# Kernel optimization log

Hardware: AMD Instinct MI355X
Metric: run time of the kernel (lower is better)

## Reference

```python
import jax, jax.numpy as jnp
from jax import lax
import numpy as np

ARG_NAMES = ('x w1 b1 bn1_g bn1_b bn1_m bn1_v w2 b2 bn2_g bn2_b bn2_m bn2_v w3 b3 w4 b4 '
             'attn_w attn_b attn_u g0_w1 g0_b1 g0_w2 g0_b2 g1_w1 g1_b1 g1_w2 g1_b2 '
             'g2_w1 g2_b1 g2_w2 g2_b2 c_w1 c_b1 c_w2 c_b2 c_w3 c_b3 c_w4 c_b4').split()


def _conv1d(x, w, b, stride, pad):
    # x: [N, C, L], w: [O, I, K]
    y = lax.conv_general_dilated(x, w, (stride,), [(pad, pad)],
                                 dimension_numbers=('NCH', 'OIH', 'NCH'))
    return y + b[None, :, None]


def _bn(x, g, b, m, v, eps=1e-5):
    # eval-mode BatchNorm1d over channel dim of [N, C, L]
    inv = g / jnp.sqrt(v + eps)
    return (x - m[None, :, None]) * inv[None, :, None] + b[None, :, None]


def _forward(x, w1, b1, bn1_g, bn1_b, bn1_m, bn1_v, w2, b2, bn2_g, bn2_b, bn2_m, bn2_v,
             w3, b3, w4, b4, attn_w, attn_b, attn_u,
             g0_w1, g0_b1, g0_w2, g0_b2, g1_w1, g1_b1, g1_w2, g1_b2,
             g2_w1, g2_b1, g2_w2, g2_b2,
             c_w1, c_b1, c_w2, c_b2, c_w3, c_b3, c_w4, c_b4):
    B, S, C, T = x.shape  # [batch, crops, channels=64, time=400]
    h = x.reshape(-1, C, T)
    # CNN stack (dropout = identity in eval)
    h = _bn(jax.nn.elu(_conv1d(h, w1, b1, 2, 1)), bn1_g, bn1_b, bn1_m, bn1_v)   # [N,64,192]
    h = _bn(jax.nn.elu(_conv1d(h, w2, b2, 2, 0)), bn2_g, bn2_b, bn2_m, bn2_v)   # [N,64,87]
    h = jax.nn.elu(_conv1d(h, w3, b3, 1, 0))                                    # [N,64,82]
    h = lax.reduce_window(h, 0.0, lax.add, (1, 1, 3), (1, 1, 2), 'VALID') / 3.0  # [N,64,40]
    h = jax.nn.elu(_conv1d(h, w4, b4, 1, 0))                                    # [N,64,35]
    h = h.reshape(B, S, C, -1)  # [B, S, 64, 35]
    # Attention pooling over the crop dim (dim=1), sum=True
    v = jnp.tanh(jnp.einsum('bsch,hd->bscd', h, attn_w) + attn_b)
    alphas = jax.nn.softmax(jnp.einsum('bscd,d->bsc', v, attn_u), axis=1)
    h = jax.nn.elu((h * alphas[..., None]).sum(axis=1))  # [B, 64, 35]
    # GIN over complete 64-node graph (self-loops included, eps=0):
    # aggregation per node == sum over all nodes of the graph
    def gin(h, W1, B1, W2, B2):
        agg = h + h.sum(axis=1, keepdims=True)
        return jax.nn.relu(agg @ W1 + B1) @ W2 + B2
    h = jax.nn.relu(gin(h, g0_w1, g0_b1, g0_w2, g0_b2))
    h = jax.nn.relu(gin(h, g1_w1, g1_b1, g1_w2, g1_b2))
    h = gin(h, g2_w1, g2_b1, g2_w2, g2_b2)  # no act after last layer
    # Classifier
    f = h.reshape(B, -1)  # [B, 2240]
    f = jax.nn.elu(f @ c_w1 + c_b1)
    f = jax.nn.elu(f @ c_w2 + c_b2)
    f = jax.nn.elu(f @ c_w3 + c_b3)
    return f @ c_w4 + c_b4  # [B, 2]


def setup_inputs() -> dict:
    key = jax.random.key(0)
    ks = iter(jax.random.split(key, 64))
    def rn(shape, s=0.05):
        return jax.random.normal(next(ks), shape, dtype=jnp.float32) * s
    d = {}
    d['x'] = jax.random.normal(next(ks), (32, 16, 64, 400), dtype=jnp.float32)
    d['w1'] = rn((64, 64, 20)); d['b1'] = rn((64,))
    d['bn1_g'] = jnp.ones((64,), jnp.float32); d['bn1_b'] = jnp.zeros((64,), jnp.float32)
    d['bn1_m'] = jnp.zeros((64,), jnp.float32); d['bn1_v'] = jnp.ones((64,), jnp.float32)
    d['w2'] = rn((64, 64, 20)); d['b2'] = rn((64,))
    d['bn2_g'] = jnp.ones((64,), jnp.float32); d['bn2_b'] = jnp.zeros((64,), jnp.float32)
    d['bn2_m'] = jnp.zeros((64,), jnp.float32); d['bn2_v'] = jnp.ones((64,), jnp.float32)
    d['w3'] = rn((64, 64, 6)); d['b3'] = rn((64,))
    d['w4'] = rn((64, 64, 6)); d['b4'] = rn((64,))
    d['attn_w'] = rn((35, 256), 0.1); d['attn_b'] = rn((256,), 0.1); d['attn_u'] = rn((256,), 0.1)
    d['g0_w1'] = rn((35, 256)); d['g0_b1'] = rn((256,))
    d['g0_w2'] = rn((256, 256)); d['g0_b2'] = rn((256,))
    d['g1_w1'] = rn((256, 256)); d['g1_b1'] = rn((256,))
    d['g1_w2'] = rn((256, 256)); d['g1_b2'] = rn((256,))
    d['g2_w1'] = rn((256, 35)); d['g2_b1'] = rn((35,))
    d['g2_w2'] = rn((35, 35)); d['g2_b2'] = rn((35,))
    d['c_w1'] = rn((2240, 256)); d['c_b1'] = rn((256,))
    d['c_w2'] = rn((256, 64)); d['c_b2'] = rn((64,))
    d['c_w3'] = rn((64, 16)); d['c_b3'] = rn((16,))
    d['c_w4'] = rn((16, 2)); d['c_b4'] = rn((2,))
    return d


def reference(x, w1, b1, bn1_g, bn1_b, bn1_m, bn1_v, w2, b2, bn2_g, bn2_b, bn2_m, bn2_v,
              w3, b3, w4, b4, attn_w, attn_b, attn_u,
              g0_w1, g0_b1, g0_w2, g0_b2, g1_w1, g1_b1, g1_w2, g1_b2,
              g2_w1, g2_b1, g2_w2, g2_b2,
              c_w1, c_b1, c_w2, c_b2, c_w3, c_b3, c_w4, c_b4):
    return _forward(x, w1, b1, bn1_g, bn1_b, bn1_m, bn1_v, w2, b2, bn2_g, bn2_b, bn2_m, bn2_v,
                    w3, b3, w4, b4, attn_w, attn_b, attn_u,
                    g0_w1, g0_b1, g0_w2, g0_b2, g1_w1, g1_b1, g1_w2, g1_b2,
                    g2_w1, g2_b1, g2_w2, g2_b2,
                    c_w1, c_b1, c_w2, c_b2, c_w3, c_b3, c_w4, c_b4)
```

## Files before the change

kernel.cpp:

```cpp
#include <hip/hip_runtime.h>
#include <math.h>

typedef __attribute__((ext_vector_type(8))) __bf16 bf16x8;
typedef __attribute__((ext_vector_type(4))) __bf16 bf16x4;
typedef __attribute__((ext_vector_type(4))) float f32x4;

__device__ __forceinline__ float elu_f(float v) {
    return v > 0.f ? v : (expf(v) - 1.f);
}

__global__ __launch_bounds__(256) void prep_all(
    const float* __restrict__ w1, const float* __restrict__ w2,
    const float* __restrict__ w3, const float* __restrict__ w4,
    __bf16* __restrict__ t1, __bf16* __restrict__ t2,
    __bf16* __restrict__ t3, __bf16* __restrict__ t4,
    const float* __restrict__ g0w1, const float* __restrict__ g0w2,
    const float* __restrict__ g1w1, const float* __restrict__ g1w2,
    const float* __restrict__ g2w1, const float* __restrict__ g2w2,
    __bf16* __restrict__ d0, __bf16* __restrict__ d1, __bf16* __restrict__ d2,
    __bf16* __restrict__ d3, __bf16* __restrict__ d4, __bf16* __restrict__ d5)
{
    __shared__ float tl[64][68];
    const int bigbid = blockIdx.x;
    if (bigbid < 832) {
        int idx = bigbid * 256 + threadIdx.x;
        if (idx < 81920) {
            int k = idx / 4096, r = idx - k * 4096, co = r >> 6, ci = r & 63;
            t1[idx] = (__bf16)w1[(co * 64 + ci) * 20 + k];
        } else if (idx < 163840) {
            int j = idx - 81920;
            int k = j / 4096, r = j - k * 4096, co = r >> 6, ci = r & 63;
            t2[j] = (__bf16)w2[(co * 64 + ci) * 20 + k];
        } else if (idx < 188416) {
            int j = idx - 163840;
            int k = j / 4096, r = j - k * 4096, co = r >> 6, ci = r & 63;
            t3[j] = (__bf16)w3[(co * 64 + ci) * 6 + k];
        } else if (idx < 212992) {
            int j = idx - 188416;
            int k = j / 4096, r = j - k * 4096, co = r >> 6, ci = r & 63;
            t4[j] = (__bf16)w4[(co * 64 + ci) * 6 + k];
        }
        return;
    }
    int bid = bigbid - 832;
    const float* src; __bf16* dst; int K, O, Kpad, Opad, tile;
    if (bid < 4)       { src = g0w1; dst = d0; K = 35;   O = 256; Kpad = 64;   Opad = 256; tile = bid; }
    else if (bid < 20) { src = g0w2; dst = d1; K = 256;  O = 256; Kpad = 256;  Opad = 256; tile = bid - 4; }
    else if (bid < 36) { src = g1w1; dst = d2; K = 256;  O = 256; Kpad = 256;  Opad = 256; tile = bid - 20; }
    else if (bid < 52) { src = g1w2; dst = d3; K = 256;  O = 256; Kpad = 256;  Opad = 256; tile = bid - 36; }
    else if (bid < 56) { src = g2w1; dst = d4; K = 256;  O = 35;  Kpad = 256;  Opad = 64;  tile = bid - 52; }
    else               { src = g2w2; dst = d5; K = 35;   O = 35;  Kpad = 64;   Opad = 64;  tile = 0; }
    int ktiles = Kpad >> 6;
    int ot = tile / ktiles, kt = tile - ot * ktiles;
    int k0 = kt * 64, o0 = ot * 64;
    size_t LOFF = (size_t)Opad * Kpad;
    int c = threadIdx.x & 63, rr = threadIdx.x >> 6;
    #pragma unroll
    for (int it = 0; it < 16; ++it) {
        int r = rr + it * 4;
        int kk = k0 + r, oo = o0 + c;
        tl[r][c] = (kk < K && oo < O) ? src[(size_t)kk * O + oo] : 0.f;
    }
    __syncthreads();
    #pragma unroll
    for (int it = 0; it < 16; ++it) {
        int r = rr + it * 4;
        float v = tl[c][r];
        __bf16 hi = (__bf16)v;
        float lo = v - (float)hi;
        size_t pos = (size_t)(o0 + r) * Kpad + k0 + c;
        dst[pos] = hi;
        dst[LOFF + pos] = (__bf16)lo;
    }
}

__global__ __launch_bounds__(512, 2) void conv1234_fused(
    const float* __restrict__ x, const __bf16* __restrict__ wT1,
    const float* __restrict__ b1,
    const float* __restrict__ bn1g, const float* __restrict__ bn1b,
    const float* __restrict__ bn1m, const float* __restrict__ bn1v,
    const __bf16* __restrict__ wT2, const float* __restrict__ b2,
    const float* __restrict__ bn2g, const float* __restrict__ bn2b,
    const float* __restrict__ bn2m, const float* __restrict__ bn2v,
    const __bf16* __restrict__ wT3, const float* __restrict__ b3,
    const __bf16* __restrict__ wT4, const float* __restrict__ b4,
    __bf16* __restrict__ h4)
{
    constexpr int LIN = 400, PAD = 1;
    constexpr int ROWS = 201;
    __shared__ __align__(16) __bf16 smem[2 * ROWS * 72];
    __shared__ __align__(16) __bf16 sw[2 * 64 * 72];

    __bf16* sx   = smem;
    __bf16* bufA = smem;
    __bf16* bufB = smem + 2 * 96 * 72;

    const int tid = threadIdx.x;
    const int n = blockIdx.x;
    const int wave = tid >> 6, lane = tid & 63;
    const int m = lane & 15, quad = lane >> 4;

    {
        const float* xg = x + (size_t)n * 64 * LIN;
        if (tid < 128) {
            int v = (tid >> 6) ? 401 : 0;
            sx[((v & 1) * ROWS + (v >> 1)) * 72 + (tid & 63)] = (__bf16)0.f;
        }
        constexpr int ITEMS = 16 * (LIN / 4);
        #pragma unroll
        for (int it = 0; it < 4; ++it) {
            int idx = it * 512 + tid;
            if (idx < ITEMS) {
                int jj = idx & 3;
                int g  = (idx >> 2) & 15;
                int q  = (idx >> 6) * 4 + jj;
                const float* xp = xg + (size_t)(4 * g) * LIN + 4 * q;
                float fa[4][4];
                #pragma unroll
                for (int u = 0; u < 4; ++u)
                    *(float4*)&fa[u][0] = *(const float4*)(xp + (size_t)u * LIN);
                #pragma unroll
                for (int e = 0; e < 4; ++e) {
                    int v = 4 * q + e + PAD;
                    bf16x4 wv = { (__bf16)fa[0][e], (__bf16)fa[1][e],
                                  (__bf16)fa[2][e], (__bf16)fa[3][e] };
                    *(bf16x4*)&sx[((v & 1) * ROWS + (v >> 1)) * 72 + 4 * g] = wv;
                }
            }
        }
    }

    const int tile = wave >> 1;
    const int coh  = (wave & 1) * 32;
    {
        f32x4 acc[3][2];
        #pragma unroll
        for (int mi = 0; mi < 3; ++mi)
            #pragma unroll
            for (int nj = 0; nj < 2; ++nj)
                acc[mi][nj] = (f32x4){0.f, 0.f, 0.f, 0.f};

        for (int kb = 0; kb < 20; kb += 2) {
            if (kb) __syncthreads();
            #pragma unroll
            for (int i = 0; i < 2; ++i) {
                int idx = i * 512 + tid;
                int r = idx >> 3, p = idx & 7;
                *(uint4*)(sw + (size_t)r * 72 + p * 8) =
                    *(const uint4*)(wT1 + (size_t)(kb + (r >> 6)) * 4096 + (r & 63) * 64 + p * 8);
            }
            __syncthreads();

            #pragma unroll
            for (int kp2 = 0; kp2 < 2; ++kp2) {
                const int kp = kb + kp2;
                const int buf = kp & 1, rowoff = kp >> 1;
                const __bf16* abase = sx + ((size_t)buf * ROWS + tile * 48 + m + rowoff) * 72;
                const __bf16* bbase = sw + (size_t)(kp2 * 64 + coh + m) * 72;
                #pragma unroll
                for (int s = 0; s < 2; ++s) {
                    bf16x8 af[3], bfr[2];
                    #pragma unroll
                    for (int mi = 0; mi < 3; ++mi)
                        af[mi] = *(const bf16x8*)(abase + mi * (16 * 72) + s * 32 + quad * 8);
                    #pragma unroll
                    for (int nj = 0; nj < 2; ++nj)
                        bfr[nj] = *(const bf16x8*)(bbase + nj * (16 * 72) + s * 32 + quad * 8);
                    #pragma unroll
                    for (int mi = 0; mi < 3; ++mi)
                        #pragma unroll
                        for (int nj = 0; nj < 2; ++nj)
                            acc[mi][nj] = __builtin_amdgcn_mfma_f32_16x16x32_bf16(
                                af[mi], bfr[nj], acc[mi][nj], 0, 0, 0);
                }
            }
        }
        __syncthreads();

        #pragma unroll
        for (int nj = 0; nj < 2; ++nj) {
            const int co = coh + nj * 16 + m;
            const float bi = b1[co];
            const float inv   = bn1g[co] / sqrtf(bn1v[co] + 1e-5f);
            const float shift = bn1b[co] - bn1m[co] * inv;
            #pragma unroll
            for (int mi = 0; mi < 3; ++mi)
                #pragma unroll
                for (int r = 0; r < 4; ++r) {
                    int t = tile * 48 + mi * 16 + quad * 4 + r;
                    float v = elu_f(acc[mi][nj][r] + bi) * inv + shift;
                    bufA[((size_t)(t & 1) * 96 + (t >> 1)) * 72 + co] = (__bf16)v;
                }
        }
    }
    __syncthreads();

    const int th  = wave >> 2;
    const int coq = wave & 3;
    {
        f32x4 acc[3];
        #pragma unroll
        for (int mi = 0; mi < 3; ++mi) acc[mi] = (f32x4){0.f, 0.f, 0.f, 0.f};

        for (int kb = 0; kb < 20; kb += 2) {
            __syncthreads();
            #pragma unroll
            for (int i = 0; i < 2; ++i) {
                int idx = i * 512 + tid;
                int r = idx >> 3, p = idx & 7;
                *(uint4*)(sw + (size_t)r * 72 + p * 8) =
                    *(const uint4*)(wT2 + (size_t)(kb + (r >> 6)) * 4096 + (r & 63) * 64 + p * 8);
            }
            __syncthreads();

            #pragma unroll
            for (int kp2 = 0; kp2 < 2; ++kp2) {
                const int kp = kb + kp2;
                const int buf = kp & 1, rowoff = kp >> 1;
                const int r0 = th * 48 + m + rowoff;
                const __bf16* bbase = sw + (size_t)(kp2 * 64 + coq * 16 + m) * 72;
                #pragma unroll
                for (int s = 0; s < 2; ++s) {
                    bf16x8 af[3], bfr;
                    #pragma unroll
                    for (int mi = 0; mi < 3; ++mi) {
                        int rr = r0 + mi * 16; if (rr > 95) rr = 95;
                        af[mi] = *(const bf16x8*)(bufA + ((size_t)buf * 96 + rr) * 72 + s * 32 + quad * 8);
                    }
                    bfr = *(const bf16x8*)(bbase + s * 32 + quad * 8);
                    #pragma unroll
                    for (int mi = 0; mi < 3; ++mi)
                        acc[mi] = __builtin_amdgcn_mfma_f32_16x16x32_bf16(
                            af[mi], bfr, acc[mi], 0, 0, 0);
                }
            }
        }

        const int co = coq * 16 + m;
        const float bi = b2[co];
        float inv = bn2g[co] / sqrtf(bn2v[co] + 1e-5f);
        float shift = bn2b[co] - bn2m[co] * inv;
        #pragma unroll
        for (int mi = 0; mi < 3; ++mi)
            #pragma unroll
            for (int r = 0; r < 4; ++r) {
                int t = th * 48 + mi * 16 + quad * 4 + r;
                if (t < 87) {
                    float v = elu_f(acc[mi][r] + bi) * inv + shift;
                    bufB[t * 72 + co] = (__bf16)v;
                }
            }
    }
    __syncthreads();

    {
        const __bf16* wb = wT3 + (size_t)(coq * 16 + m) * 64 + quad * 8;
        bf16x8 bw[6][2];
        #pragma unroll
        for (int kp = 0; kp < 6; ++kp)
            #pragma unroll
            for (int s = 0; s < 2; ++s)
                bw[kp][s] = *(const bf16x8*)(wb + (size_t)kp * 4096 + s * 32);

        f32x4 acc[3];
        #pragma unroll
        for (int mi = 0; mi < 3; ++mi) acc[mi] = (f32x4){0.f, 0.f, 0.f, 0.f};

        #pragma unroll
        for (int kp = 0; kp < 6; ++kp) {
            const int r0 = th * 48 + m + kp;
            #pragma unroll
            for (int s = 0; s < 2; ++s) {
                bf16x8 af[3];
                #pragma unroll
                for (int mi = 0; mi < 3; ++mi) {
                    int rr = r0 + mi * 16; if (rr > 86) rr = 86;
                    af[mi] = *(const bf16x8*)(bufB + (size_t)rr * 72 + s * 32 + quad * 8);
                }
                #pragma unroll
                for (int mi = 0; mi < 3; ++mi)
                    acc[mi] = __builtin_amdgcn_mfma_f32_16x16x32_bf16(
                        af[mi], bw[kp][s], acc[mi], 0, 0, 0);
            }
        }

        const int co = coq * 16 + m;
        const float bi = b3[co];
        #pragma unroll
        for (int mi = 0; mi < 3; ++mi)
            #pragma unroll
            for (int r = 0; r < 4; ++r) {
                int t = th * 48 + mi * 16 + quad * 4 + r;
                if (t < 82)
                    bufA[(size_t)t * 72 + co] = (__bf16)elu_f(acc[mi][r] + bi);
            }
    }
    __syncthreads();

    #pragma unroll
    for (int it = 0; it < 5; ++it) {
        int idx = it * 512 + tid;
        int t = idx >> 6, co = idx & 63;
        float v = ((float)bufA[(2 * t) * 72 + co] + (float)bufA[(2 * t + 1) * 72 + co] +
                   (float)bufA[(2 * t + 2) * 72 + co]) * (1.f / 3.f);
        bufB[t * 72 + co] = (__bf16)v;
    }
    __syncthreads();

    if (wave < 4) {
        const int co0 = wave * 16;
        const __bf16* wb = wT4 + (size_t)(co0 + m) * 64 + quad * 8;
        bf16x8 bw[6][2];
        #pragma unroll
        for (int kp = 0; kp < 6; ++kp)
            #pragma unroll
            for (int s = 0; s < 2; ++s)
                bw[kp][s] = *(const bf16x8*)(wb + (size_t)kp * 4096 + s * 32);

        f32x4 acc4[3];
        #pragma unroll
        for (int mi = 0; mi < 3; ++mi) acc4[mi] = (f32x4){0.f, 0.f, 0.f, 0.f};

        #pragma unroll
        for (int kp = 0; kp < 6; ++kp) {
            const int r0 = m + kp;
            #pragma unroll
            for (int s = 0; s < 2; ++s) {
                bf16x8 af[3];
                #pragma unroll
                for (int mi = 0; mi < 3; ++mi) {
                    int rr = r0 + mi * 16; if (rr > 39) rr = 39;
                    af[mi] = *(const bf16x8*)(bufB + (size_t)rr * 72 + s * 32 + quad * 8);
                }
                #pragma unroll
                for (int mi = 0; mi < 3; ++mi)
                    acc4[mi] = __builtin_amdgcn_mfma_f32_16x16x32_bf16(
                        af[mi], bw[kp][s], acc4[mi], 0, 0, 0);
            }
        }

        const int co = co0 + m;
        const float bi = b4[co];
        #pragma unroll
        for (int mi = 0; mi < 3; ++mi)
            #pragma unroll
            for (int r = 0; r < 4; ++r) {
                int t = mi * 16 + quad * 4 + r;
                if (t < 35)
                    h4[((size_t)n * 35 + t) * 64 + co] = (__bf16)elu_f(acc4[mi][r] + bi);
            }
    }
}

__global__ __launch_bounds__(256) void attn_pool_k(
    const __bf16* __restrict__ h, const float* __restrict__ W,
    const float* __restrict__ ab, const float* __restrict__ u,
    float* __restrict__ out)
{
    __shared__ float sW[35 * 256];
    __shared__ float sh[4][16 * 35 + 5];
    const int tid = threadIdx.x;
    const int pair0 = blockIdx.x * 4;
    for (int i = tid; i < 35 * 256; i += 256) sW[i] = W[i];
    for (int i = tid; i < 4 * 560; i += 256) {
        int q = i / 560, r = i - q * 560;
        int s = r / 35, t = r - s * 35;
        int bc = pair0 + q, b = bc >> 6, c = bc & 63;
        sh[q][s * 35 + t] = (float)h[(((size_t)b * 16 + s) * 35 + t) * 64 + c];
    }
    __syncthreads();

    const int wave = tid >> 6, lane = tid & 63;
    const int bc = pair0 + wave;
    const float* shw = sh[wave];

    float myu[4], myb[4];
    #pragma unroll
    for (int p = 0; p < 4; ++p) { myu[p] = u[lane + 64 * p]; myb[p] = ab[lane + 64 * p]; }

    float dot[16][4];
    #pragma unroll
    for (int s = 0; s < 16; ++s)
        #pragma unroll
        for (int p = 0; p < 4; ++p) dot[s][p] = myb[p];

    for (int t = 0; t < 35; ++t) {
        float w0 = sW[t * 256 + lane];
        float w1 = sW[t * 256 + lane + 64];
        float w2 = sW[t * 256 + lane + 128];
        float w3 = sW[t * 256 + lane + 192];
        #pragma unroll
        for (int s = 0; s < 16; ++s) {
            float hv = shw[s * 35 + t];
            dot[s][0] = fmaf(hv, w0, dot[s][0]);
            dot[s][1] = fmaf(hv, w1, dot[s][1]);
            dot[s][2] = fmaf(hv, w2, dot[s][2]);
            dot[s][3] = fmaf(hv, w3, dot[s][3]);
        }
    }

    float sc[16];
    #pragma unroll
    for (int s = 0; s < 16; ++s) {
        float v = tanhf(dot[s][0]) * myu[0] + tanhf(dot[s][1]) * myu[1]
                + tanhf(dot[s][2]) * myu[2] + tanhf(dot[s][3]) * myu[3];
        #pragma unroll
        for (int off = 1; off < 64; off <<= 1) v += __shfl_xor(v, off, 64);
        sc[s] = v;
    }

    float mx = sc[0];
    #pragma unroll
    for (int s = 1; s < 16; ++s) mx = fmaxf(mx, sc[s]);
    float e[16], sum = 0.f;
    #pragma unroll
    for (int s = 0; s < 16; ++s) { e[s] = expf(sc[s] - mx); sum += e[s]; }
    float inv = 1.f / sum;

    if (lane < 35) {
        float acc = 0.f;
        #pragma unroll
        for (int s = 0; s < 16; ++s) acc = fmaf(shw[s * 35 + lane], e[s] * inv, acc);
        out[(size_t)bc * 35 + lane] = elu_f(acc);
    }
}

#define APLANE (64 * 264)

__device__ __forceinline__ void gin_gemm_dev(
    const __bf16* As,
    const __bf16* __restrict__ Wg, int Kpad, int wlo, int Kout,
    const float* __restrict__ bias,
    int mode, __bf16* Ad, float* __restrict__ outg)
{
    const int lane = threadIdx.x & 63;
    const int wave = threadIdx.x >> 6;
    const int o0 = wave * 32;
    if (o0 >= ((Kout + 63) & ~63)) return;
    const int m = lane & 15, quad = lane >> 4;

    f32x4 acc[4][2];
    #pragma unroll
    for (int mi = 0; mi < 4; ++mi)
        #pragma unroll
        for (int nj = 0; nj < 2; ++nj)
            acc[mi][nj] = (f32x4){0.f, 0.f, 0.f, 0.f};

    for (int k0 = 0; k0 < Kpad; k0 += 32) {
        bf16x8 ah[4], al[4], bh[2], bl[2];
        #pragma unroll
        for (int mi = 0; mi < 4; ++mi) {
            const __bf16* ap = As + (size_t)(mi * 16 + m) * 264 + k0 + quad * 8;
            ah[mi] = *(const bf16x8*)ap;
            al[mi] = *(const bf16x8*)(ap + APLANE);
        }
        #pragma unroll
        for (int nj = 0; nj < 2; ++nj) {
            const __bf16* wp = Wg + (size_t)(o0 + nj * 16 + m) * Kpad + k0 + quad * 8;
            bh[nj] = *(const bf16x8*)wp;
            bl[nj] = *(const bf16x8*)(wp + wlo);
        }
        #pragma unroll
        for (int mi = 0; mi < 4; ++mi)
            #pragma unroll
            for (int nj = 0; nj < 2; ++nj) {
                acc[mi][nj] = __builtin_amdgcn_mfma_f32_16x16x32_bf16(
                    al[mi], bh[nj], acc[mi][nj], 0, 0, 0);
                acc[mi][nj] = __builtin_amdgcn_mfma_f32_16x16x32_bf16(
                    ah[mi], bl[nj], acc[mi][nj], 0, 0, 0);
                acc[mi][nj] = __builtin_amdgcn_mfma_f32_16x16x32_bf16(
                    ah[mi], bh[nj], acc[mi][nj], 0, 0, 0);
            }
    }

    #pragma unroll
    for (int nj = 0; nj < 2; ++nj) {
        const int o = o0 + nj * 16 + m;
        const bool ovalid = (o < Kout);
        const float bi = ovalid ? bias[o] : 0.f;
        float v[4][4];
        #pragma unroll
        for (int mi = 0; mi < 4; ++mi)
            #pragma unroll
            for (int r = 0; r < 4; ++r)
                v[mi][r] = acc[mi][nj][r] + bi;
        if (mode == 2) {
            if (ovalid) {
                #pragma unroll
                for (int mi = 0; mi < 4; ++mi)
                    #pragma unroll
                    for (int r = 0; r < 4; ++r)
                        outg[(size_t)(mi * 16 + quad * 4 + r) * Kout + o] = v[mi][r];
            }
        } else {
            float s = 0.f;
            #pragma unroll
            for (int mi = 0; mi < 4; ++mi)
                #pragma unroll
                for (int r = 0; r < 4; ++r) {
                    float rv = ovalid ? fmaxf(v[mi][r], 0.f) : 0.f;
                    v[mi][r] = rv;
                    s += rv;
                }
            if (mode == 1) {
                s += __shfl_xor(s, 16, 64);
                s += __shfl_xor(s, 32, 64);
            } else {
                s = 0.f;
            }
            #pragma unroll
            for (int mi = 0; mi < 4; ++mi)
                #pragma unroll
                for (int r = 0; r < 4; ++r) {
                    float a = v[mi][r] + s;
                    __bf16 hi = (__bf16)a;
                    size_t pos = (size_t)(mi * 16 + quad * 4 + r) * 264 + o;
                    Ad[pos] = hi;
                    Ad[APLANE + pos] = (__bf16)(a - (float)hi);
                }
        }
    }
}

__global__ __launch_bounds__(512) void gin_fused(
    const float* __restrict__ ha,
    const __bf16* __restrict__ gW0a, const __bf16* __restrict__ gW0b,
    const __bf16* __restrict__ gW1a, const __bf16* __restrict__ gW1b,
    const __bf16* __restrict__ gW2a, const __bf16* __restrict__ gW2b,
    const float* __restrict__ b0a, const float* __restrict__ b0b,
    const float* __restrict__ b1a, const float* __restrict__ b1b,
    const float* __restrict__ b2a, const float* __restrict__ b2b,
    float* __restrict__ H3)
{
    const int b = blockIdx.x, tid = threadIdx.x;
    __shared__ __align__(16) __bf16 sA[2][2 * APLANE];
    __shared__ float sS[64];
    const float* hab = ha + (size_t)b * 2240;

    if (tid < 64) {
        float s = 0.f;
        if (tid < 35)
            for (int n = 0; n < 64; ++n) s += hab[n * 35 + tid];
        sS[tid] = s;
    }
    __syncthreads();
    for (int idx = tid; idx < 64 * 64; idx += 512) {
        int n = idx >> 6, k = idx & 63;
        float a = (k < 35) ? hab[n * 35 + k] + sS[k] : 0.f;
        __bf16 hi = (__bf16)a;
        sA[0][n * 264 + k] = hi;
        sA[0][APLANE + n * 264 + k] = (__bf16)(a - (float)hi);
    }
    __syncthreads();

    gin_gemm_dev(sA[0], gW0a, 64,  16384, 256, b0a, 0, sA[1], nullptr); __syncthreads();
    gin_gemm_dev(sA[1], gW0b, 256, 65536, 256, b0b, 1, sA[0], nullptr); __syncthreads();
    gin_gemm_dev(sA[0], gW1a, 256, 65536, 256, b1a, 0, sA[1], nullptr); __syncthreads();
    gin_gemm_dev(sA[1], gW1b, 256, 65536, 256, b1b, 1, sA[0], nullptr); __syncthreads();
    gin_gemm_dev(sA[0], gW2a, 256, 16384, 35,  b2a, 0, sA[1], nullptr); __syncthreads();
    gin_gemm_dev(sA[1], gW2b, 64,  4096,  35,  b2b, 2, nullptr, H3 + (size_t)b * 2240);
}

__global__ __launch_bounds__(256) void cls1_part_k(
    const float* __restrict__ H3, const float* __restrict__ w1,
    float* __restrict__ s1p)
{
    const int b  = blockIdx.x;
    const int kc = blockIdx.y;
    const int k0 = kc * 140;
    __shared__ float sH[140];
    const int tid = threadIdx.x;
    if (tid < 140) sH[tid] = H3[(size_t)b * 2240 + k0 + tid];
    __syncthreads();
    const int o = (tid >> 6) * 64 + (tid & 63);
    float a0 = 0.f, a1 = 0.f, a2 = 0.f, a3 = 0.f;
    const float* wr = w1 + (size_t)k0 * 256 + o;
    #pragma unroll
    for (int k = 0; k < 140; k += 4) {
        a0 = fmaf(sH[k],     wr[(size_t)k * 256],       a0);
        a1 = fmaf(sH[k + 1], wr[(size_t)(k + 1) * 256], a1);
        a2 = fmaf(sH[k + 2], wr[(size_t)(k + 2) * 256], a2);
        a3 = fmaf(sH[k + 3], wr[(size_t)(k + 3) * 256], a3);
    }
    s1p[((size_t)kc * 32 + b) * 256 + o] = a0 + a1 + a2 + a3;
}

__global__ __launch_bounds__(256) void cls234_k(
    const float* __restrict__ s1p, const float* __restrict__ b1,
    const float* __restrict__ w2, const float* __restrict__ b2,
    const float* __restrict__ w3, const float* __restrict__ b3,
    const float* __restrict__ w4, const float* __restrict__ b4,
    float* __restrict__ out)
{
    const int b = blockIdx.x, tid = threadIdx.x;
    __shared__ float s1[256];
    __shared__ float part[4][64];
    __shared__ float s2[64];
    __shared__ float s3[16];
    {
        float acc = b1[tid];
        #pragma unroll
        for (int kc = 0; kc < 16; ++kc)
            acc += s1p[((size_t)kc * 32 + b) * 256 + tid];
        s1[tid] = elu_f(acc);
    }
    __syncthreads();
    {
        int kg = tid >> 6, o = tid & 63;
        float acc = 0.f;
        for (int k = kg * 64; k < kg * 64 + 64; ++k)
            acc = fmaf(s1[k], w2[k * 64 + o], acc);
        part[kg][o] = acc;
    }
    __syncthreads();
    if (tid < 64) {
        float acc = part[0][tid] + part[1][tid] + part[2][tid] + part[3][tid] + b2[tid];
        s2[tid] = elu_f(acc);
    }
    __syncthreads();
    if (tid < 16) {
        float acc = b3[tid];
        for (int k = 0; k < 64; ++k) acc = fmaf(s2[k], w3[k * 16 + tid], acc);
        s3[tid] = elu_f(acc);
    }
    __syncthreads();
    if (tid < 2) {
        float acc = b4[tid];
        for (int k = 0; k < 16; ++k) acc = fmaf(s3[k], w4[k * 2 + tid], acc);
        out[b * 2 + tid] = acc;
    }
}

extern "C" void kernel_launch(void* const* d_in, const int* in_sizes, int n_in,
                              void* d_out, int out_size, void* d_ws, size_t ws_size,
                              hipStream_t stream)
{
    const float* x     = (const float*)d_in[0];
    const float* w1    = (const float*)d_in[1];
    const float* b1    = (const float*)d_in[2];
    const float* bn1_g = (const float*)d_in[3];
    const float* bn1_b = (const float*)d_in[4];
    const float* bn1_m = (const float*)d_in[5];
    const float* bn1_v = (const float*)d_in[6];
    const float* w2    = (const float*)d_in[7];
    const float* b2    = (const float*)d_in[8];
    const float* bn2_g = (const float*)d_in[9];
    const float* bn2_b = (const float*)d_in[10];
    const float* bn2_m = (const float*)d_in[11];
    const float* bn2_v = (const float*)d_in[12];
    const float* w3    = (const float*)d_in[13];
    const float* b3    = (const float*)d_in[14];
    const float* w4    = (const float*)d_in[15];
    const float* b4    = (const float*)d_in[16];
    const float* attn_w = (const float*)d_in[17];
    const float* attn_b = (const float*)d_in[18];
    const float* attn_u = (const float*)d_in[19];
    const float* g0_w1 = (const float*)d_in[20];
    const float* g0_b1 = (const float*)d_in[21];
    const float* g0_w2 = (const float*)d_in[22];
    const float* g0_b2 = (const float*)d_in[23];
    const float* g1_w1 = (const float*)d_in[24];
    const float* g1_b1 = (const float*)d_in[25];
    const float* g1_w2 = (const float*)d_in[26];
    const float* g1_b2 = (const float*)d_in[27];
    const float* g2_w1 = (const float*)d_in[28];
    const float* g2_b1 = (const float*)d_in[29];
    const float* g2_w2 = (const float*)d_in[30];
    const float* g2_b2 = (const float*)d_in[31];
    const float* c_w1  = (const float*)d_in[32];
    const float* c_b1  = (const float*)d_in[33];
    const float* c_w2  = (const float*)d_in[34];
    const float* c_b2  = (const float*)d_in[35];
    const float* c_w3  = (const float*)d_in[36];
    const float* c_b3  = (const float*)d_in[37];
    const float* c_w4  = (const float*)d_in[38];
    const float* c_b4  = (const float*)d_in[39];
    float* out = (float*)d_out;

    char* ws = (char*)d_ws;
    __bf16* wT1  = (__bf16*)(ws + 0);
    __bf16* wT2  = (__bf16*)(ws + 163840);
    __bf16* wT3  = (__bf16*)(ws + 327680);
    __bf16* wT4  = (__bf16*)(ws + 376832);
    __bf16* h4   = (__bf16*)(ws + 13008896);
    float*  ha   = (float*)(ws + 15302656);
    __bf16* gW0a = (__bf16*)(ws + 15589376);
    __bf16* gW0b = (__bf16*)(ws + 15654912);
    __bf16* gW1a = (__bf16*)(ws + 15917056);
    __bf16* gW1b = (__bf16*)(ws + 16179200);
    __bf16* gW2a = (__bf16*)(ws + 16441344);
    __bf16* gW2b = (__bf16*)(ws + 16506880);
    float*  H3   = (float*)(ws + 16523264);
    float*  s1p  = (float*)(ws + 16809984);

    prep_all<<<dim3(889), dim3(256), 0, stream>>>(
        w1, w2, w3, w4, wT1, wT2, wT3, wT4,
        g0_w1, g0_w2, g1_w1, g1_w2, g2_w1, g2_w2,
        gW0a, gW0b, gW1a, gW1b, gW2a, gW2b);

    conv1234_fused<<<dim3(512), dim3(512), 0, stream>>>(
        x, wT1, b1, bn1_g, bn1_b, bn1_m, bn1_v,
        wT2, b2, bn2_g, bn2_b, bn2_m, bn2_v,
        wT3, b3, wT4, b4, h4);

    attn_pool_k<<<dim3(512), dim3(256), 0, stream>>>(h4, attn_w, attn_b, attn_u, ha);

    gin_fused<<<dim3(32), dim3(512), 0, stream>>>(
        ha, gW0a, gW0b, gW1a, gW1b, gW2a, gW2b,
        g0_b1, g0_b2, g1_b1, g1_b2, g2_b1, g2_b2, H3);

    cls1_part_k<<<dim3(32, 16), dim3(256), 0, stream>>>(H3, c_w1, s1p);
    cls234_k<<<dim3(32), dim3(256), 0, stream>>>(s1p, c_b1, c_w2, c_b2, c_w3, c_b3,
                                                 c_w4, c_b4, out);
}
```

Before: 282.4 us.

## Fuse attention pooling, GIN and classifier into one per-batch tail kernel

Replaces four kernel launches (attention pooling, GIN, classifier layer-1 partials, classifier tail) with a single 32-block kernel that keeps intermediates in shared memory. It removes launch gaps and global round-trips for the pooled features, GIN output and partial sums. In exchange, attention pooling and the 2240x256 classifier GEMV now run on only 32 blocks instead of 512. Each block processes 64 channels sequentially, which cuts parallelism sharply.

```diff
diff --git a/kernel.cpp b/kernel.cpp
--- a/kernel.cpp
+++ b/kernel.cpp
@@ -352,86 +352,13 @@
     }
 }
 
-__global__ __launch_bounds__(256) void attn_pool_k(
-    const __bf16* __restrict__ h, const float* __restrict__ W,
-    const float* __restrict__ ab, const float* __restrict__ u,
-    float* __restrict__ out)
-{
-    __shared__ float sW[35 * 256];
-    __shared__ float sh[4][16 * 35 + 5];
-    const int tid = threadIdx.x;
-    const int pair0 = blockIdx.x * 4;
-    for (int i = tid; i < 35 * 256; i += 256) sW[i] = W[i];
-    for (int i = tid; i < 4 * 560; i += 256) {
-        int q = i / 560, r = i - q * 560;
-        int s = r / 35, t = r - s * 35;
-        int bc = pair0 + q, b = bc >> 6, c = bc & 63;
-        sh[q][s * 35 + t] = (float)h[(((size_t)b * 16 + s) * 35 + t) * 64 + c];
-    }
-    __syncthreads();
-
-    const int wave = tid >> 6, lane = tid & 63;
-    const int bc = pair0 + wave;
-    const float* shw = sh[wave];
-
-    float myu[4], myb[4];
-    #pragma unroll
-    for (int p = 0; p < 4; ++p) { myu[p] = u[lane + 64 * p]; myb[p] = ab[lane + 64 * p]; }
-
-    float dot[16][4];
-    #pragma unroll
-    for (int s = 0; s < 16; ++s)
-        #pragma unroll
-        for (int p = 0; p < 4; ++p) dot[s][p] = myb[p];
-
-    for (int t = 0; t < 35; ++t) {
-        float w0 = sW[t * 256 + lane];
-        float w1 = sW[t * 256 + lane + 64];
-        float w2 = sW[t * 256 + lane + 128];
-        float w3 = sW[t * 256 + lane + 192];
-        #pragma unroll
-        for (int s = 0; s < 16; ++s) {
-            float hv = shw[s * 35 + t];
-            dot[s][0] = fmaf(hv, w0, dot[s][0]);
-            dot[s][1] = fmaf(hv, w1, dot[s][1]);
-            dot[s][2] = fmaf(hv, w2, dot[s][2]);
-            dot[s][3] = fmaf(hv, w3, dot[s][3]);
-        }
-    }
-
-    float sc[16];
-    #pragma unroll
-    for (int s = 0; s < 16; ++s) {
-        float v = tanhf(dot[s][0]) * myu[0] + tanhf(dot[s][1]) * myu[1]
-                + tanhf(dot[s][2]) * myu[2] + tanhf(dot[s][3]) * myu[3];
-        #pragma unroll
-        for (int off = 1; off < 64; off <<= 1) v += __shfl_xor(v, off, 64);
-        sc[s] = v;
-    }
-
-    float mx = sc[0];
-    #pragma unroll
-    for (int s = 1; s < 16; ++s) mx = fmaxf(mx, sc[s]);
-    float e[16], sum = 0.f;
-    #pragma unroll
-    for (int s = 0; s < 16; ++s) { e[s] = expf(sc[s] - mx); sum += e[s]; }
-    float inv = 1.f / sum;
-
-    if (lane < 35) {
-        float acc = 0.f;
-        #pragma unroll
-        for (int s = 0; s < 16; ++s) acc = fmaf(shw[s * 35 + lane], e[s] * inv, acc);
-        out[(size_t)bc * 35 + lane] = elu_f(acc);
-    }
-}
-
 #define APLANE (64 * 264)
 
 __device__ __forceinline__ void gin_gemm_dev(
     const __bf16* As,
     const __bf16* __restrict__ Wg, int Kpad, int wlo, int Kout,
     const float* __restrict__ bias,
-    int mode, __bf16* Ad, float* __restrict__ outg)
+    int mode, __bf16* Ad, float* outg)
 {
     const int lane = threadIdx.x & 63;
     const int wave = threadIdx.x >> 6;
@@ -522,31 +449,113 @@
     }
 }
 
-__global__ __launch_bounds__(512) void gin_fused(
-    const float* __restrict__ ha,
+__global__ __launch_bounds__(512) void tail_fused(
+    const __bf16* __restrict__ h4,
+    const float* __restrict__ W, const float* __restrict__ ab,
+    const float* __restrict__ u,
     const __bf16* __restrict__ gW0a, const __bf16* __restrict__ gW0b,
     const __bf16* __restrict__ gW1a, const __bf16* __restrict__ gW1b,
     const __bf16* __restrict__ gW2a, const __bf16* __restrict__ gW2b,
     const float* __restrict__ b0a, const float* __restrict__ b0b,
     const float* __restrict__ b1a, const float* __restrict__ b1b,
     const float* __restrict__ b2a, const float* __restrict__ b2b,
-    float* __restrict__ H3)
+    const float* __restrict__ cw1, const float* __restrict__ cb1,
+    const float* __restrict__ cw2, const float* __restrict__ cb2,
+    const float* __restrict__ cw3, const float* __restrict__ cb3,
+    const float* __restrict__ cw4, const float* __restrict__ cb4,
+    float* __restrict__ out)
 {
     const int b = blockIdx.x, tid = threadIdx.x;
+    const int wave = tid >> 6, lane = tid & 63;
+
     __shared__ __align__(16) __bf16 sA[2][2 * APLANE];
+    __shared__ float haL[2240];
     __shared__ float sS[64];
-    const float* hab = ha + (size_t)b * 2240;
+    __shared__ float s1[256];
+    __shared__ float part[4][64];
+    __shared__ float s2[64];
+    __shared__ float s3[16];
+
+    float* sW = (float*)&sA[0][0];
+    __bf16* h4s = (__bf16*)((char*)&sA[0][0] + 35840);
+    for (int i = tid; i < 35 * 256; i += 512) sW[i] = W[i];
+    {
+        const __bf16* src = h4 + (size_t)b * 560 * 64;
+        for (int idx = tid; idx < 4480; idx += 512) {
+            int r = idx >> 3, p = idx & 7;
+            *(uint4*)(h4s + (size_t)r * 72 + p * 8) =
+                *(const uint4*)(src + (size_t)r * 64 + p * 8);
+        }
+    }
+    __syncthreads();
+
+    {
+        float myu[4], myb[4];
+        #pragma unroll
+        for (int p = 0; p < 4; ++p) { myu[p] = u[lane + 64 * p]; myb[p] = ab[lane + 64 * p]; }
+
+        for (int cc = 0; cc < 8; ++cc) {
+            const int c = wave * 8 + cc;
+            float dot[16][4];
+            #pragma unroll
+            for (int s = 0; s < 16; ++s)
+                #pragma unroll
+                for (int p = 0; p < 4; ++p) dot[s][p] = myb[p];
+
+            for (int t = 0; t < 35; ++t) {
+                float w0 = sW[t * 256 + lane];
+                float w1v = sW[t * 256 + lane + 64];
+                float w2v = sW[t * 256 + lane + 128];
+                float w3v = sW[t * 256 + lane + 192];
+                #pragma unroll
+                for (int s = 0; s < 16; ++s) {
+                    float hv = (float)h4s[(size_t)(s * 35 + t) * 72 + c];
+                    dot[s][0] = fmaf(hv, w0, dot[s][0]);
+                    dot[s][1] = fmaf(hv, w1v, dot[s][1]);
+                    dot[s][2] = fmaf(hv, w2v, dot[s][2]);
+                    dot[s][3] = fmaf(hv, w3v, dot[s][3]);
+                }
+            }
+
+            float sc[16];
+            #pragma unroll
+            for (int s = 0; s < 16; ++s) {
+                float v = tanhf(dot[s][0]) * myu[0] + tanhf(dot[s][1]) * myu[1]
+                        + tanhf(dot[s][2]) * myu[2] + tanhf(dot[s][3]) * myu[3];
+                #pragma unroll
+                for (int off = 1; off < 64; off <<= 1) v += __shfl_xor(v, off, 64);
+                sc[s] = v;
+            }
+
+            float mx = sc[0];
+            #pragma unroll
+            for (int s = 1; s < 16; ++s) mx = fmaxf(mx, sc[s]);
+            float e[16], sum = 0.f;
+            #pragma unroll
+            for (int s = 0; s < 16; ++s) { e[s] = expf(sc[s] - mx); sum += e[s]; }
+            float inv = 1.f / sum;
+
+            if (lane < 35) {
+                float acc = 0.f;
+                #pragma unroll
+                for (int s = 0; s < 16; ++s)
+                    acc = fmaf((float)h4s[(size_t)(s * 35 + lane) * 72 + c], e[s] * inv, acc);
+                haL[c * 35 + lane] = elu_f(acc);
+            }
+        }
+    }
+    __syncthreads();
 
     if (tid < 64) {
         float s = 0.f;
         if (tid < 35)
-            for (int n = 0; n < 64; ++n) s += hab[n * 35 + tid];
+            for (int n = 0; n < 64; ++n) s += haL[n * 35 + tid];
         sS[tid] = s;
     }
     __syncthreads();
     for (int idx = tid; idx < 64 * 64; idx += 512) {
         int n = idx >> 6, k = idx & 63;
-        float a = (k < 35) ? hab[n * 35 + k] + sS[k] : 0.f;
+        float a = (k < 35) ? haL[n * 35 + k] + sS[k] : 0.f;
         __bf16 hi = (__bf16)a;
         sA[0][n * 264 + k] = hi;
         sA[0][APLANE + n * 264 + k] = (__bf16)(a - (float)hi);
@@ -558,75 +567,50 @@
     gin_gemm_dev(sA[0], gW1a, 256, 65536, 256, b1a, 0, sA[1], nullptr); __syncthreads();
     gin_gemm_dev(sA[1], gW1b, 256, 65536, 256, b1b, 1, sA[0], nullptr); __syncthreads();
     gin_gemm_dev(sA[0], gW2a, 256, 16384, 35,  b2a, 0, sA[1], nullptr); __syncthreads();
-    gin_gemm_dev(sA[1], gW2b, 64,  4096,  35,  b2b, 2, nullptr, H3 + (size_t)b * 2240);
-}
-
-__global__ __launch_bounds__(256) void cls1_part_k(
-    const float* __restrict__ H3, const float* __restrict__ w1,
-    float* __restrict__ s1p)
-{
-    const int b  = blockIdx.x;
-    const int kc = blockIdx.y;
-    const int k0 = kc * 140;
-    __shared__ float sH[140];
-    const int tid = threadIdx.x;
-    if (tid < 140) sH[tid] = H3[(size_t)b * 2240 + k0 + tid];
-    __syncthreads();
-    const int o = (tid >> 6) * 64 + (tid & 63);
-    float a0 = 0.f, a1 = 0.f, a2 = 0.f, a3 = 0.f;
-    const float* wr = w1 + (size_t)k0 * 256 + o;
-    #pragma unroll
-    for (int k = 0; k < 140; k += 4) {
-        a0 = fmaf(sH[k],     wr[(size_t)k * 256],       a0);
-        a1 = fmaf(sH[k + 1], wr[(size_t)(k + 1) * 256], a1);
-        a2 = fmaf(sH[k + 2], wr[(size_t)(k + 2) * 256], a2);
-        a3 = fmaf(sH[k + 3], wr[(size_t)(k + 3) * 256], a3);
-    }
-    s1p[((size_t)kc * 32 + b) * 256 + o] = a0 + a1 + a2 + a3;
-}
-
-__global__ __launch_bounds__(256) void cls234_k(
-    const float* __restrict__ s1p, const float* __restrict__ b1,
-    const float* __restrict__ w2, const float* __restrict__ b2,
-    const float* __restrict__ w3, const float* __restrict__ b3,
-    const float* __restrict__ w4, const float* __restrict__ b4,
-    float* __restrict__ out)
-{
-    const int b = blockIdx.x, tid = threadIdx.x;
-    __shared__ float s1[256];
-    __shared__ float part[4][64];
-    __shared__ float s2[64];
-    __shared__ float s3[16];
-    {
-        float acc = b1[tid];
-        #pragma unroll
-        for (int kc = 0; kc < 16; ++kc)
-            acc += s1p[((size_t)kc * 32 + b) * 256 + tid];
+    gin_gemm_dev(sA[1], gW2b, 64,  4096,  35,  b2b, 2, nullptr, haL);
+    __syncthreads();
+
+    if (tid < 256) {
+        float acc = cb1[tid];
+        for (int kc = 0; kc < 16; ++kc) {
+            const int k0 = kc * 140;
+            float a0 = 0.f, a1 = 0.f, a2 = 0.f, a3 = 0.f;
+            const float* wr = cw1 + (size_t)k0 * 256 + tid;
+            #pragma unroll
+            for (int k = 0; k < 140; k += 4) {
+                a0 = fmaf(haL[k0 + k],     wr[(size_t)k * 256],       a0);
+                a1 = fmaf(haL[k0 + k + 1], wr[(size_t)(k + 1) * 256], a1);
+                a2 = fmaf(haL[k0 + k + 2], wr[(size_t)(k + 2) * 256], a2);
+                a3 = fmaf(haL[k0 + k + 3], wr[(size_t)(k + 3) * 256], a3);
+            }
+            acc += a0 + a1 + a2 + a3;
+        }
         s1[tid] = elu_f(acc);
     }
     __syncthreads();
-    {
+
+    if (tid < 256) {
         int kg = tid >> 6, o = tid & 63;
         float acc = 0.f;
         for (int k = kg * 64; k < kg * 64 + 64; ++k)
-            acc = fmaf(s1[k], w2[k * 64 + o], acc);
+            acc = fmaf(s1[k], cw2[k * 64 + o], acc);
         part[kg][o] = acc;
     }
     __syncthreads();
     if (tid < 64) {
-        float acc = part[0][tid] + part[1][tid] + part[2][tid] + part[3][tid] + b2[tid];
+        float acc = part[0][tid] + part[1][tid] + part[2][tid] + part[3][tid] + cb2[tid];
         s2[tid] = elu_f(acc);
     }
     __syncthreads();
     if (tid < 16) {
-        float acc = b3[tid];
-        for (int k = 0; k < 64; ++k) acc = fmaf(s2[k], w3[k * 16 + tid], acc);
+        float acc = cb3[tid];
+        for (int k = 0; k < 64; ++k) acc = fmaf(s2[k], cw3[k * 16 + tid], acc);
         s3[tid] = elu_f(acc);
     }
     __syncthreads();
     if (tid < 2) {
-        float acc = b4[tid];
-        for (int k = 0; k < 16; ++k) acc = fmaf(s3[k], w4[k * 2 + tid], acc);
+        float acc = cb4[tid];
+        for (int k = 0; k < 16; ++k) acc = fmaf(s3[k], cw4[k * 2 + tid], acc);
         out[b * 2 + tid] = acc;
     }
 }
@@ -683,15 +667,12 @@
     __bf16* wT3  = (__bf16*)(ws + 327680);
     __bf16* wT4  = (__bf16*)(ws + 376832);
     __bf16* h4   = (__bf16*)(ws + 13008896);
-    float*  ha   = (float*)(ws + 15302656);
     __bf16* gW0a = (__bf16*)(ws + 15589376);
     __bf16* gW0b = (__bf16*)(ws + 15654912);
     __bf16* gW1a = (__bf16*)(ws + 15917056);
     __bf16* gW1b = (__bf16*)(ws + 16179200);
     __bf16* gW2a = (__bf16*)(ws + 16441344);
     __bf16* gW2b = (__bf16*)(ws + 16506880);
-    float*  H3   = (float*)(ws + 16523264);
-    float*  s1p  = (float*)(ws + 16809984);
 
     prep_all<<<dim3(889), dim3(256), 0, stream>>>(
         w1, w2, w3, w4, wT1, wT2, wT3, wT4,
@@ -703,13 +684,9 @@
         wT2, b2, bn2_g, bn2_b, bn2_m, bn2_v,
         wT3, b3, wT4, b4, h4);
 
-    attn_pool_k<<<dim3(512), dim3(256), 0, stream>>>(h4, attn_w, attn_b, attn_u, ha);
-
-    gin_fused<<<dim3(32), dim3(512), 0, stream>>>(
-        ha, gW0a, gW0b, gW1a, gW1b, gW2a, gW2b,
-        g0_b1, g0_b2, g1_b1, g1_b2, g2_b1, g2_b2, H3);
-
-    cls1_part_k<<<dim3(32, 16), dim3(256), 0, stream>>>(H3, c_w1, s1p);
-    cls234_k<<<dim3(32), dim3(256), 0, stream>>>(s1p, c_b1, c_w2, c_b2, c_w3, c_b3,
-                                                 c_w4, c_b4, out);
+    tail_fused<<<dim3(32), dim3(512), 0, stream>>>(
+        h4, attn_w, attn_b, attn_u,
+        gW0a, gW0b, gW1a, gW1b, gW2a, gW2b,
+        g0_b1, g0_b2, g1_b1, g1_b2, g2_b1, g2_b2,
+        c_w1, c_b1, c_w2, c_b2, c_w3, c_b3, c_w4, c_b4, out);
 }
```

New measurement: 626.8 us. 122% more time.
